# Performance work log

Hardware: AMD Instinct MI355X
Metric: run time of the kernel (lower is better)

Reference implementation:

```python
import jax, jax.numpy as jnp
import numpy as np

B, S, D = 1, 2048, 2048
H, KV, HD = 32, 8, 64
POWER = 100000.0


def _rotary(x):
    # x: [B, h, S, HD]; faithful to RotaryEncoder: freqs = pos / div_term
    rot_dim = HD // 2
    pos = jnp.arange(S, dtype=x.dtype)
    div = POWER ** (jnp.arange(0, HD, 2, dtype=x.dtype) / HD)  # [HD//2]
    freqs = pos[:, None] / div  # [S, HD//2]
    cos, sin = jnp.cos(freqs), jnp.sin(freqs)
    x_rot, x_pass = x[..., :rot_dim], x[..., rot_dim:]
    h = rot_dim // 2
    rot_half = jnp.concatenate([-x_rot[..., h:], x_rot[..., :h]], axis=-1)
    return jnp.concatenate([x_rot * cos + rot_half * sin, x_pass], axis=-1)


def setup_inputs() -> dict:
    key = jax.random.key(0)
    k1, k2, k3 = jax.random.split(key, 3)
    hidden_states = jax.random.normal(k1, (B, S, D), dtype=jnp.float32)
    op_size = H * HD + 2 * KV * HD
    Wqkv = jax.random.normal(k2, (D, op_size), dtype=jnp.float32) * 0.02
    Wo = jax.random.normal(k3, (H * HD, D), dtype=jnp.float32) * 0.02
    causal = jnp.tril(jnp.ones((S, S), dtype=bool))
    attention_mask = jnp.where(causal, 0.0, -1e9).astype(jnp.float32)[None, None]
    return {"hidden_states": hidden_states, "attention_mask": attention_mask,
            "Wqkv": Wqkv, "Wo": Wo}


def reference(hidden_states, attention_mask, Wqkv, Wo):
    groups = H // KV
    qkv = hidden_states @ Wqkv  # [B, S, op_size]
    qpos = H * HD
    q = qkv[..., :qpos].reshape(B, S, H, HD).transpose(0, 2, 1, 3)
    k = qkv[..., qpos:qpos + KV * HD].reshape(B, S, KV, HD).transpose(0, 2, 1, 3)
    v = qkv[..., qpos + KV * HD:].reshape(B, S, KV, HD).transpose(0, 2, 1, 3)
    q = _rotary(q)
    k = _rotary(k)
    k = jnp.repeat(k, groups, axis=1)  # GQA repeat_interleave -> [B, H, S, HD]
    v = jnp.repeat(v, groups, axis=1)
    scores = jnp.einsum('bhqd,bhkd->bhqk', q, k) / jnp.sqrt(jnp.float32(HD))
    scores = scores + attention_mask[..., :S]
    attn = jax.nn.softmax(scores.astype(jnp.float32), axis=-1).astype(v.dtype)
    out = jnp.einsum('bhqk,bhkd->bhqd', attn, v)
    out = out.transpose(0, 2, 1, 3).reshape(B, S, H * HD)
    return out @ Wo
```

## Files before the change

kernel.cpp:

```cpp
#include <hip/hip_runtime.h>
#include <hip/hip_bf16.h>
#include <cstdint>
#include <cstddef>

#define S_LEN 2048
#define D_MODEL 2048
#define NH 32
#define NKV 8
#define HDIM 64
#define OPSZ 3072
#define KOFF 2048
#define VOFF 2560

typedef float    floatx4 __attribute__((ext_vector_type(4)));
typedef __bf16   bf16x8  __attribute__((ext_vector_type(8)));
typedef __bf16   bf16x4  __attribute__((ext_vector_type(4)));
typedef __bf16   bf16_t;
typedef _Float16 f16_t;
typedef _Float16 f16x4   __attribute__((ext_vector_type(4)));
typedef _Float16 f16x8   __attribute__((ext_vector_type(8)));

__device__ __forceinline__ void gld16(const void* g, void* l) {
  __builtin_amdgcn_global_load_lds((__attribute__((address_space(1))) void*)(void*)g,
                                   (__attribute__((address_space(3))) void*)l,
                                   16, 0, 0);
}

__global__ __launch_bounds__(256)
void prep_kernel(const float* __restrict__ X, const float* __restrict__ Wqkv,
                 const float* __restrict__ Wo, bf16_t* __restrict__ Xb,
                 bf16_t* __restrict__ WqkvT, bf16_t* __restrict__ WoT) {
  const int bx = blockIdx.x;
  const int k0 = blockIdx.y * 32;
  const int tx = threadIdx.x & 31, ty = threadIdx.x >> 5;
  if (bx < 160) {
    __shared__ float tile[32][33];
    const float* W; bf16_t* Wt; int N, n0;
    if (bx < 96) { W = Wqkv; Wt = WqkvT; N = OPSZ;    n0 = bx * 32; }
    else         { W = Wo;   Wt = WoT;   N = D_MODEL; n0 = (bx - 96) * 32; }
#pragma unroll
    for (int i = 0; i < 32; i += 8)
      tile[ty + i][tx] = W[(size_t)(k0 + ty + i) * N + n0 + tx];
    __syncthreads();
#pragma unroll
    for (int i = 0; i < 32; i += 8)
      Wt[(size_t)(n0 + ty + i) * D_MODEL + k0 + tx] = (bf16_t)tile[tx][ty + i];
  } else {
    const int n0 = (bx - 160) * 32;
#pragma unroll
    for (int i = 0; i < 32; i += 8) {
      const size_t idx = (size_t)(k0 + ty + i) * D_MODEL + n0 + tx;
      Xb[idx] = (bf16_t)X[idx];
    }
  }
}

#define GEMM64_CORE(A_, Bt_, K_, m0_, n0_)                                        \
  const int tid = threadIdx.x;                                                    \
  const int wave = tid >> 6;                                                      \
  const int lane = tid & 63;                                                      \
  const int lane15 = lane & 15;                                                   \
  const int quad = lane >> 4;                                                     \
  const int wm = (wave & 1) * 32;                                                 \
  const int wn = (wave >> 1) * 64;                                                \
  floatx4 acc[2][4];                                                              \
  _Pragma("unroll") for (int i = 0; i < 2; i++)                                   \
    _Pragma("unroll") for (int j = 0; j < 4; j++)                                 \
      acc[i][j] = floatx4{0.f, 0.f, 0.f, 0.f};                                    \
  {                                                                               \
     \
    int arow[4], acol[4], apan[4];                                                \
    _Pragma("unroll") for (int i = 0; i < 4; i++) {                               \
      const int c = tid + i * 256;                                                \
      apan[i] = c >> 8; arow[i] = (c & 255) >> 2; acol[i] = (c & 3) * 8;          \
    }                                                                             \
                            \
    int brow[8], bcol[8], bpan[8];                                                \
    _Pragma("unroll") for (int i = 0; i < 8; i++) {                               \
      const int c = tid + i * 256;                                                \
      bpan[i] = c >> 9; brow[i] = (c & 511) >> 2; bcol[i] = (c & 3) * 8;          \
    }                                                                             \
    for (int k0 = 0; k0 < (K_); k0 += 128) {                                      \
      __syncthreads();                                                            \
      _Pragma("unroll") for (int i = 0; i < 4; i++)                               \
        gld16((A_) + (size_t)((m0_) + arow[i]) * (K_) + k0 + apan[i] * 32 + acol[i], \
              &As[(i * 256 + wave * 64) * 8]);                                    \
      _Pragma("unroll") for (int i = 0; i < 8; i++)                               \
        gld16((Bt_) + (size_t)((n0_) + brow[i]) * (K_) + k0 + bpan[i] * 32 + bcol[i], \
              &Bs[(i * 256 + wave * 64) * 8]);                                    \
      __syncthreads();                                                            \
      _Pragma("unroll") for (int kt = 0; kt < 4; kt++) {                          \
        bf16x8 af[2], bfr[4];                                                     \
        _Pragma("unroll") for (int mi = 0; mi < 2; mi++)                          \
          af[mi] = *(const bf16x8*)&As[kt * 2048 + (wm + mi * 16 + lane15) * 32 + quad * 8]; \
        _Pragma("unroll") for (int ni = 0; ni < 4; ni++)                          \
          bfr[ni] = *(const bf16x8*)&Bs[kt * 4096 + (wn + ni * 16 + lane15) * 32 + quad * 8]; \
        _Pragma("unroll") for (int mi = 0; mi < 2; mi++)                          \
          _Pragma("unroll") for (int ni = 0; ni < 4; ni++)                        \
            acc[mi][ni] = __builtin_amdgcn_mfma_f32_16x16x32_bf16(af[mi], bfr[ni],\
                                                                  acc[mi][ni], 0, 0, 0); \
      }                                                                           \
    }                                                                             \
  }

#define QSCALE 0.18033688011112042f
__global__ __launch_bounds__(256, 3)
void gemm_qkv_rope(const bf16_t* __restrict__ A, const bf16_t* __restrict__ Bt,
                   bf16_t* __restrict__ Qr, bf16_t* __restrict__ Kr,
                   f16_t* __restrict__ VtG) {
  __shared__ bf16_t As[4 * 64 * 32];
  __shared__ bf16_t Bs[4 * 128 * 32];
  const int m0 = blockIdx.y * 64;
  const int n0 = blockIdx.x * 128;
  GEMM64_CORE(A, Bt, D_MODEL, m0, n0)

  const int colbase = n0 + wn;
  const int s0 = m0 + wm;

  if (colbase < VOFF) {
    const bool isQ = (colbase < KOFF);
    const float k2 = 0.51905126483f;
    const float pj0 = exp2f(-(float)lane15 * k2);
    const float pj1 = pj0 * 0.0031622776601684f;
    bf16_t* dst = isQ ? (Qr + ((size_t)(colbase >> 6) * S_LEN) * HDIM)
                      : (Kr + ((size_t)((colbase - KOFF) >> 6) * S_LEN) * HDIM);
    const float qs = isQ ? QSCALE : 1.0f;
#pragma unroll
    for (int mi = 0; mi < 2; mi++) {
#pragma unroll
      for (int r = 0; r < 4; r++) {
        const int s = s0 + mi * 16 + quad * 4 + r;
        const float sf = (float)s;
        float s0s, s0c, s1s, s1c;
        __sincosf(sf * pj0, &s0s, &s0c);
        __sincosf(sf * pj1, &s1s, &s1c);
        const float x0 = acc[mi][0][r], x1 = acc[mi][1][r];
        bf16_t* row = dst + (size_t)s * HDIM + lane15;
        row[0]  = (bf16_t)((x0 * s0c - x1 * s0s) * qs);
        row[16] = (bf16_t)((x1 * s1c + x0 * s1s) * qs);
        row[32] = (bf16_t)(acc[mi][2][r] * qs);
        row[48] = (bf16_t)(acc[mi][3][r] * qs);
      }
    }
  } else {
    const int kvv = (colbase - VOFF) >> 6;
    f16_t* dst = VtG + (size_t)kvv * HDIM * S_LEN;
#pragma unroll
    for (int mi = 0; mi < 2; mi++) {
      const int s = s0 + mi * 16 + quad * 4;
#pragma unroll
      for (int ni = 0; ni < 4; ni++) {
        const int d = ni * 16 + lane15;
        f16x4 tv;
#pragma unroll
        for (int r = 0; r < 4; r++) tv[r] = (f16_t)acc[mi][ni][r];
        *(f16x4*)&dst[(size_t)d * S_LEN + s] = tv;
      }
    }
  }
}

__global__ __launch_bounds__(256, 3)
void gemm_bt_f32out(const bf16_t* __restrict__ A, const bf16_t* __restrict__ Bt,
                    float* __restrict__ C, int M, int N, int K) {
  __shared__ bf16_t As[4 * 64 * 32];
  __shared__ bf16_t Bs[4 * 128 * 32];
  const int m0 = blockIdx.y * 64;
  const int n0 = blockIdx.x * 128;
  GEMM64_CORE(A, Bt, K, m0, n0)

#pragma unroll
  for (int mi = 0; mi < 2; mi++)
#pragma unroll
    for (int r = 0; r < 4; r++) {
      const int row = m0 + wm + mi * 16 + quad * 4 + r;
#pragma unroll
      for (int ni = 0; ni < 4; ni++) {
        const int col = n0 + wn + ni * 16 + lane15;
        C[(size_t)row * N + col] = acc[mi][ni][r];
      }
    }
}

#define KST 72
#define VST 136
__global__ __launch_bounds__(256, 4)
void flash_kernel(const bf16_t* __restrict__ Qr, const bf16_t* __restrict__ Kr,
                  const f16_t* __restrict__ VtG, bf16_t* __restrict__ attn) {
  __shared__ bf16_t Ks[128 * KST];
  __shared__ f16_t  Vt[64 * VST];

  const int tid = threadIdx.x;
  const int wave = tid >> 6;
  const int lane = tid & 63;
  const int lane15 = lane & 15;
  const int quad = lane >> 4;
  const int bx = blockIdx.x;
  const int h = bx & 31;
  const int qblk = 31 - (bx >> 5);
  const int q0 = qblk * 64;
  const int rq = q0 + wave * 16;
  const int kv = h >> 2;
  const size_t kbase = (size_t)kv * S_LEN * HDIM;
  const size_t vbase = (size_t)kv * HDIM * S_LEN;

  const int kr_ = tid >> 3, kc_ = (tid & 7) * 8;
  const int vd_ = tid >> 4, vc_ = (tid & 15) * 8;

  bf16x8 aq[2];
#pragma unroll
  for (int kt = 0; kt < 2; kt++)
    aq[kt] = *(const bf16x8*)&Qr[((size_t)h * S_LEN + rq + lane15) * HDIM + kt * 32 + quad * 8];

  float m_run = -1e30f, l_run = 0.f;
  floatx4 o[4];
#pragma unroll
  for (int dt = 0; dt < 4; dt++) o[dt] = floatx4{0.f, 0.f, 0.f, 0.f};

  const int nk = (qblk + 2) >> 1;

  for (int t = 0; t < nk; ++t) {
    const int p0 = t * 128;
    __syncthreads();
#pragma unroll
    for (int i = 0; i < 4; i++) {
      const int r = kr_ + i * 32;
      *(bf16x8*)&Ks[r * KST + kc_] = *(const bf16x8*)&Kr[kbase + (size_t)(p0 + r) * HDIM + kc_];
    }
#pragma unroll
    for (int i = 0; i < 4; i++) {
      const int d = vd_ + i * 16;
      *(f16x8*)&Vt[d * VST + vc_] = *(const f16x8*)&VtG[vbase + (size_t)d * S_LEN + p0 + vc_];
    }
    __syncthreads();

    floatx4 sc[8];
#pragma unroll
    for (int nt = 0; nt < 8; nt++) sc[nt] = floatx4{0.f, 0.f, 0.f, 0.f};
#pragma unroll
    for (int kt = 0; kt < 2; kt++) {
#pragma unroll
      for (int nt = 0; nt < 8; nt++) {
        const bf16x8 ak = *(const bf16x8*)&Ks[(nt * 16 + lane15) * KST + kt * 32 + quad * 8];
        sc[nt] = __builtin_amdgcn_mfma_f32_16x16x32_bf16(ak, aq[kt], sc[nt], 0, 0, 0);
      }
    }

    if (p0 + 127 > rq) {
#pragma unroll
      for (int nt = 0; nt < 8; nt++)
#pragma unroll
        for (int r = 0; r < 4; r++) {
          const int kpos = p0 + nt * 16 + quad * 4 + r;
          const int qrow = rq + lane15;
          if (kpos > qrow) sc[nt][r] = -1e30f;
        }
    }

    float mt = fmaxf(fmaxf(sc[0][0], sc[0][1]), fmaxf(sc[0][2], sc[0][3]));
#pragma unroll
    for (int nt = 1; nt < 8; nt++)
#pragma unroll
      for (int r = 0; r < 4; r++) mt = fmaxf(mt, sc[nt][r]);
    mt = fmaxf(mt, __shfl_xor(mt, 16));
    mt = fmaxf(mt, __shfl_xor(mt, 32));
    const float mnew = fmaxf(m_run, mt);
    const float alpha = exp2f(m_run - mnew);
    m_run = mnew;
    float rs = 0.f;
    f16x4 ph[8];
#pragma unroll
    for (int nt = 0; nt < 8; nt++) {
      f16x4 pv;
#pragma unroll
      for (int r = 0; r < 4; r++) {
        const float p = exp2f(sc[nt][r] - mnew);
        rs += p;
        pv[r] = (f16_t)p;
      }
      ph[nt] = pv;
    }
    rs += __shfl_xor(rs, 16);
    rs += __shfl_xor(rs, 32);
    l_run = l_run * alpha + rs;
#pragma unroll
    for (int dt = 0; dt < 4; dt++)
#pragma unroll
      for (int r = 0; r < 4; r++) o[dt][r] *= alpha;

#pragma unroll
    for (int kt4 = 0; kt4 < 8; kt4++) {
#pragma unroll
      for (int dt = 0; dt < 4; dt++) {
        const f16x4 av = *(const f16x4*)&Vt[(dt * 16 + lane15) * VST + kt4 * 16 + quad * 4];
        o[dt] = __builtin_amdgcn_mfma_f32_16x16x16f16(av, ph[kt4], o[dt], 0, 0, 0);
      }
    }
  }

  const float inv = 1.0f / l_run;
  const int s = rq + lane15;
#pragma unroll
  for (int dt = 0; dt < 4; dt++) {
    bf16x4 tv;
#pragma unroll
    for (int r = 0; r < 4; r++) tv[r] = (bf16_t)(o[dt][r] * inv);
    *(bf16x4*)&attn[(size_t)s * D_MODEL + h * HDIM + dt * 16 + quad * 4] = tv;
  }
}

extern "C" void kernel_launch(void* const* d_in, const int* in_sizes, int n_in,
                              void* d_out, int out_size, void* d_ws, size_t ws_size,
                              hipStream_t stream) {
  (void)in_sizes; (void)n_in; (void)out_size; (void)ws_size;
  const float* hidden = (const float*)d_in[0];
  const float* Wqkv = (const float*)d_in[2];
  const float* Wo   = (const float*)d_in[3];
  float* out = (float*)d_out;

  char* ws = (char*)d_ws;
  size_t off = 0;
  auto alloc = [&](size_t bytes) -> void* {
    void* p = ws + off;
    off += (bytes + 255) & ~(size_t)255;
    return p;
  };
  bf16_t* Xb    = (bf16_t*)alloc((size_t)S_LEN * D_MODEL * 2);
  bf16_t* WqkvT = (bf16_t*)alloc((size_t)OPSZ * D_MODEL * 2);
  bf16_t* WoT   = (bf16_t*)alloc((size_t)D_MODEL * D_MODEL * 2);
  bf16_t* Qr    = (bf16_t*)alloc((size_t)NH * S_LEN * HDIM * 2);
  bf16_t* Kr    = (bf16_t*)alloc((size_t)NKV * S_LEN * HDIM * 2);
  f16_t*  VtG   = (f16_t*) alloc((size_t)NKV * HDIM * S_LEN * 2);
  bf16_t* attn  = (bf16_t*)alloc((size_t)S_LEN * D_MODEL * 2);

  prep_kernel<<<dim3(224, 64), 256, 0, stream>>>(hidden, Wqkv, Wo, Xb, WqkvT, WoT);
  gemm_qkv_rope<<<dim3(OPSZ / 128, S_LEN / 64), 256, 0, stream>>>(Xb, WqkvT, Qr, Kr, VtG);
  flash_kernel<<<dim3(32 * NH), 256, 0, stream>>>(Qr, Kr, VtG, attn);
  gemm_bt_f32out<<<dim3(D_MODEL / 128, S_LEN / 64), 256, 0, stream>>>(attn, WoT, out, S_LEN, D_MODEL, D_MODEL);
}
```

Measured before the change: 215.5 us.

## Load K/V fragments directly from global memory and compute row sums via MFMA

Removes the shared-memory staging of K and V tiles and the two block barriers per iteration, so each wave reads its MFMA operands straight from global memory (relying on L1/L2 reuse across the four waves). The softmax row-sum is computed with an extra MFMA against a ones vector instead of shuffles, and exponentials use the raw hardware exp2 with packed fp16 conversion. This trades LDS traffic and synchronisation for redundant global loads per wave and possible latency exposure, and the round-toward-zero packing slightly changes rounding.

```diff
diff --git a/kernel.cpp b/kernel.cpp
--- a/kernel.cpp
+++ b/kernel.cpp
@@ -17,8 +17,10 @@
 typedef __bf16   bf16x4  __attribute__((ext_vector_type(4)));
 typedef __bf16   bf16_t;
 typedef _Float16 f16_t;
+typedef _Float16 f16x2   __attribute__((ext_vector_type(2)));
 typedef _Float16 f16x4   __attribute__((ext_vector_type(4)));
 typedef _Float16 f16x8   __attribute__((ext_vector_type(8)));
+typedef __fp16   hfx2    __attribute__((ext_vector_type(2)));
 
 __device__ __forceinline__ void gld16(const void* g, void* l) {
   __builtin_amdgcn_global_load_lds((__attribute__((address_space(1))) void*)(void*)g,
@@ -182,14 +184,9 @@
     }
 }
 
-#define KST 72
-#define VST 136
 __global__ __launch_bounds__(256, 4)
 void flash_kernel(const bf16_t* __restrict__ Qr, const bf16_t* __restrict__ Kr,
                   const f16_t* __restrict__ VtG, bf16_t* __restrict__ attn) {
-  __shared__ bf16_t Ks[128 * KST];
-  __shared__ f16_t  Vt[64 * VST];
-
   const int tid = threadIdx.x;
   const int wave = tid >> 6;
   const int lane = tid & 63;
@@ -201,18 +198,19 @@
   const int q0 = qblk * 64;
   const int rq = q0 + wave * 16;
   const int kv = h >> 2;
-  const size_t kbase = (size_t)kv * S_LEN * HDIM;
-  const size_t vbase = (size_t)kv * HDIM * S_LEN;
-
-  const int kr_ = tid >> 3, kc_ = (tid & 7) * 8;
-  const int vd_ = tid >> 4, vc_ = (tid & 15) * 8;
+
+  const bf16_t* kp = Kr + (size_t)kv * S_LEN * HDIM + (size_t)lane15 * HDIM + quad * 8;
+  const f16_t* vp = VtG + (size_t)kv * HDIM * S_LEN + (size_t)lane15 * S_LEN + quad * 4;
 
   bf16x8 aq[2];
 #pragma unroll
   for (int kt = 0; kt < 2; kt++)
     aq[kt] = *(const bf16x8*)&Qr[((size_t)h * S_LEN + rq + lane15) * HDIM + kt * 32 + quad * 8];
 
-  float m_run = -1e30f, l_run = 0.f;
+  const f16x4 vone = {(f16_t)1.0f, (f16_t)1.0f, (f16_t)1.0f, (f16_t)1.0f};
+
+  float m_run = -1e30f;
+  floatx4 lacc = floatx4{0.f, 0.f, 0.f, 0.f};
   floatx4 o[4];
 #pragma unroll
   for (int dt = 0; dt < 4; dt++) o[dt] = floatx4{0.f, 0.f, 0.f, 0.f};
@@ -221,18 +219,6 @@
 
   for (int t = 0; t < nk; ++t) {
     const int p0 = t * 128;
-    __syncthreads();
-#pragma unroll
-    for (int i = 0; i < 4; i++) {
-      const int r = kr_ + i * 32;
-      *(bf16x8*)&Ks[r * KST + kc_] = *(const bf16x8*)&Kr[kbase + (size_t)(p0 + r) * HDIM + kc_];
-    }
-#pragma unroll
-    for (int i = 0; i < 4; i++) {
-      const int d = vd_ + i * 16;
-      *(f16x8*)&Vt[d * VST + vc_] = *(const f16x8*)&VtG[vbase + (size_t)d * S_LEN + p0 + vc_];
-    }
-    __syncthreads();
 
     floatx4 sc[8];
 #pragma unroll
@@ -241,7 +227,7 @@
     for (int kt = 0; kt < 2; kt++) {
 #pragma unroll
       for (int nt = 0; nt < 8; nt++) {
-        const bf16x8 ak = *(const bf16x8*)&Ks[(nt * 16 + lane15) * KST + kt * 32 + quad * 8];
+        const bf16x8 ak = *(const bf16x8*)(kp + (size_t)(p0 + nt * 16) * HDIM + kt * 32);
         sc[nt] = __builtin_amdgcn_mfma_f32_16x16x32_bf16(ak, aq[kt], sc[nt], 0, 0, 0);
       }
     }
@@ -257,48 +243,48 @@
         }
     }
 
-    float mt = fmaxf(fmaxf(sc[0][0], sc[0][1]), fmaxf(sc[0][2], sc[0][3]));
-#pragma unroll
-    for (int nt = 1; nt < 8; nt++)
-#pragma unroll
-      for (int r = 0; r < 4; r++) mt = fmaxf(mt, sc[nt][r]);
+    float mt = -1e30f;
+#pragma unroll
+    for (int nt = 0; nt < 8; nt++) {
+      mt = fmaxf(fmaxf(mt, sc[nt][0]), sc[nt][1]);
+      mt = fmaxf(fmaxf(mt, sc[nt][2]), sc[nt][3]);
+    }
     mt = fmaxf(mt, __shfl_xor(mt, 16));
     mt = fmaxf(mt, __shfl_xor(mt, 32));
     const float mnew = fmaxf(m_run, mt);
-    const float alpha = exp2f(m_run - mnew);
+    const float alpha = __builtin_amdgcn_exp2f(m_run - mnew);
     m_run = mnew;
-    float rs = 0.f;
+
     f16x4 ph[8];
 #pragma unroll
     for (int nt = 0; nt < 8; nt++) {
-      f16x4 pv;
-#pragma unroll
-      for (int r = 0; r < 4; r++) {
-        const float p = exp2f(sc[nt][r] - mnew);
-        rs += p;
-        pv[r] = (f16_t)p;
-      }
-      ph[nt] = pv;
-    }
-    rs += __shfl_xor(rs, 16);
-    rs += __shfl_xor(rs, 32);
-    l_run = l_run * alpha + rs;
-#pragma unroll
-    for (int dt = 0; dt < 4; dt++)
-#pragma unroll
-      for (int r = 0; r < 4; r++) o[dt][r] *= alpha;
+      const float e0 = __builtin_amdgcn_exp2f(sc[nt][0] - mnew);
+      const float e1 = __builtin_amdgcn_exp2f(sc[nt][1] - mnew);
+      const float e2 = __builtin_amdgcn_exp2f(sc[nt][2] - mnew);
+      const float e3 = __builtin_amdgcn_exp2f(sc[nt][3] - mnew);
+      const hfx2 lo_ = __builtin_amdgcn_cvt_pkrtz(e0, e1);
+      const hfx2 hi_ = __builtin_amdgcn_cvt_pkrtz(e2, e3);
+      const f16x2 lo = __builtin_bit_cast(f16x2, lo_);
+      const f16x2 hi = __builtin_bit_cast(f16x2, hi_);
+      ph[nt] = __builtin_shufflevector(lo, hi, 0, 1, 2, 3);
+    }
+
+    lacc = lacc * alpha;
+#pragma unroll
+    for (int dt = 0; dt < 4; dt++) o[dt] = o[dt] * alpha;
 
 #pragma unroll
     for (int kt4 = 0; kt4 < 8; kt4++) {
+      lacc = __builtin_amdgcn_mfma_f32_16x16x16f16(vone, ph[kt4], lacc, 0, 0, 0);
 #pragma unroll
       for (int dt = 0; dt < 4; dt++) {
-        const f16x4 av = *(const f16x4*)&Vt[(dt * 16 + lane15) * VST + kt4 * 16 + quad * 4];
+        const f16x4 av = *(const f16x4*)(vp + (size_t)dt * 16 * S_LEN + p0 + kt4 * 16);
         o[dt] = __builtin_amdgcn_mfma_f32_16x16x16f16(av, ph[kt4], o[dt], 0, 0, 0);
       }
     }
   }
 
-  const float inv = 1.0f / l_run;
+  const float inv = 1.0f / lacc[0];
   const int s = rq + lane15;
 #pragma unroll
   for (int dt = 0; dt < 4; dt++) {
```

Result: slower. 380.4 us (+76.5%).
